# Kernel tuning notes

Hardware: AMD Instinct MI355X
Metric: run time of the kernel (lower is better)

## Reference

```python
import jax, jax.numpy as jnp
import numpy as np

N = 50000
IN_C, HID_C, OUT_C = 128, 64, 32
E = 800000
NEG_SLOPE = 0.2


def setup_inputs() -> dict:
    key = jax.random.key(0)
    ks = jax.random.split(key, 8)
    x = jax.random.normal(ks[0], (N, IN_C), dtype=jnp.float32)
    edge_index = jax.random.randint(ks[1], (2, E), 0, N, dtype=jnp.int64)
    # GATConv params (heads=1): lin weight, att_src/att_dst vectors, bias
    sc = 1.0 / np.sqrt(IN_C)
    W = jax.random.uniform(ks[2], (IN_C, HID_C), jnp.float32, -sc, sc)
    att_src = jax.random.normal(ks[3], (HID_C,), jnp.float32) * (1.0 / np.sqrt(HID_C))
    att_dst = jax.random.normal(ks[4], (HID_C,), jnp.float32) * (1.0 / np.sqrt(HID_C))
    bias_conv = jnp.zeros((HID_C,), jnp.float32)
    sl = 1.0 / np.sqrt(HID_C)
    W_lin = jax.random.uniform(ks[5], (HID_C, OUT_C), jnp.float32, -sl, sl)
    b_lin = jax.random.uniform(ks[6], (OUT_C,), jnp.float32, -sl, sl)
    return {"x": x, "edge_index": edge_index, "W": W, "att_src": att_src,
            "att_dst": att_dst, "bias_conv": bias_conv, "W_lin": W_lin, "b_lin": b_lin}


def reference(x, edge_index, W, att_src, att_dst, bias_conv, W_lin, b_lin):
    n = x.shape[0]
    h = x @ W  # [N, HID]
    # add self-loops (PyG GATConv default add_self_loops=True)
    loop = jnp.arange(n, dtype=edge_index.dtype)
    src = jnp.concatenate([edge_index[0], loop])  # [E+N]
    dst = jnp.concatenate([edge_index[1], loop])
    a_src = h @ att_src  # [N]
    a_dst = h @ att_dst
    e = jax.nn.leaky_relu(a_src[src] + a_dst[dst], NEG_SLOPE)  # [E+N]
    # segment softmax over incoming edges per destination node
    m = jax.ops.segment_max(e, dst, num_segments=n)
    e = jnp.exp(e - m[dst])
    denom = jax.ops.segment_sum(e, dst, num_segments=n)
    alpha = e / (denom[dst] + 1e-16)
    msg = alpha[:, None] * h[src]  # [E+N, HID]
    out = jax.ops.segment_sum(msg, dst, num_segments=n) + bias_conv
    out = jax.nn.relu(out)
    return out @ W_lin + b_lin
```

## Files before the change

### kernel.cpp

```cpp
#include <hip/hip_runtime.h>
#include <hip/hip_bf16.h>

#define IN_C  128
#define HID_C 64
#define OUT_C 32
#define NEG_SLOPE 0.2f
#define EPB1    8192
#define BUCKETW 64
#define RCAP    1536
#define NBKT    1024
#define CSTRIDE 16
#define XS_LD   136

typedef short bf16x8 __attribute__((ext_vector_type(8)));
typedef float f32x4  __attribute__((ext_vector_type(4)));

__device__ __forceinline__ unsigned short f2bf(float f) {
    __hip_bfloat16 h = __float2bfloat16(f);
    return *(unsigned short*)&h;
}
__device__ __forceinline__ float bflo(unsigned int u) {
    return __uint_as_float(u << 16);
}
__device__ __forceinline__ float bfhi(unsigned int u) {
    return __uint_as_float(u & 0xffff0000u);
}

__global__ __launch_bounds__(512) void gemm_bin1_kernel(
    const float* __restrict__ x, const float* __restrict__ W,
    const float* __restrict__ att_src, const float* __restrict__ att_dst,
    __hip_bfloat16* __restrict__ hb,
    float* __restrict__ a_src, float* __restrict__ a_dst,
    const int* __restrict__ ei, int E,
    int* __restrict__ bcur, unsigned* __restrict__ bucketbuf,
    int ngemm, int n_nodes)
{
    __shared__ __align__(16) unsigned char smem[52224];
    const int t = threadIdx.x;

    if ((int)blockIdx.x < ngemm) {
        unsigned short* xs = (unsigned short*)smem;
        unsigned short* wt = (unsigned short*)(smem + 34816);
        const int wv   = t >> 6;
        const int lane = t & 63;
        const int m16  = lane & 15;
        const int quad = lane >> 4;
        const int node0 = blockIdx.x * 128;
        const int nrows = min(128, n_nodes - node0);

        {
            const float4* xg = (const float4*)(x + (long)node0 * IN_C);
#pragma unroll
            for (int i = t; i < 4096; i += 512) {
                const int row = i >> 5;
                const int c4  = i & 31;
                float4 v = (row < nrows) ? xg[i] : make_float4(0.f, 0.f, 0.f, 0.f);
                ushort4 u;
                u.x = f2bf(v.x); u.y = f2bf(v.y);
                u.z = f2bf(v.z); u.w = f2bf(v.w);
                *(ushort4*)(xs + row * XS_LD + c4 * 4) = u;
            }
        }
        {
#pragma unroll
            for (int i = t; i < 2048; i += 512) {
                const int k  = i >> 4;
                const int n0 = (i & 15) * 4;
                const float4 v = *(const float4*)(W + k * HID_C + n0);
                wt[(n0 + 0) * XS_LD + k] = f2bf(v.x);
                wt[(n0 + 1) * XS_LD + k] = f2bf(v.y);
                wt[(n0 + 2) * XS_LD + k] = f2bf(v.z);
                wt[(n0 + 3) * XS_LD + k] = f2bf(v.w);
            }
        }
        __syncthreads();

        const int myrow0 = wv * 16;
        bf16x8 A[4];
#pragma unroll
        for (int k0 = 0; k0 < 4; ++k0)
            A[k0] = *(const bf16x8*)(xs + (myrow0 + m16) * XS_LD + k0 * 32 + quad * 8);

        f32x4 C[4];
#pragma unroll
        for (int c = 0; c < 4; ++c) {
            C[c] = (f32x4){0.f, 0.f, 0.f, 0.f};
#pragma unroll
            for (int k0 = 0; k0 < 4; ++k0) {
                const bf16x8 B = *(const bf16x8*)(wt + (c * 16 + m16) * XS_LD + k0 * 32 + quad * 8);
                C[c] = __builtin_amdgcn_mfma_f32_16x16x32_bf16(A[k0], B, C[c], 0, 0, 0);
            }
        }

#pragma unroll
        for (int c = 0; c < 4; ++c) {
#pragma unroll
            for (int r = 0; r < 4; ++r)
                xs[(myrow0 + quad * 4 + r) * XS_LD + c * 16 + m16] = f2bf(C[c][r]);
        }

        {
            float ps[4] = {0.f, 0.f, 0.f, 0.f};
            float pd[4] = {0.f, 0.f, 0.f, 0.f};
#pragma unroll
            for (int c = 0; c < 4; ++c) {
                const float av = att_src[c * 16 + m16];
                const float dv = att_dst[c * 16 + m16];
#pragma unroll
                for (int r = 0; r < 4; ++r) {
                    ps[r] = fmaf(C[c][r], av, ps[r]);
                    pd[r] = fmaf(C[c][r], dv, pd[r]);
                }
            }
#pragma unroll
            for (int off = 1; off <= 8; off <<= 1) {
#pragma unroll
                for (int r = 0; r < 4; ++r) {
                    ps[r] += __shfl_xor(ps[r], off, 64);
                    pd[r] += __shfl_xor(pd[r], off, 64);
                }
            }
            if (m16 == 0) {
#pragma unroll
                for (int r = 0; r < 4; ++r) {
                    const int row = myrow0 + quad * 4 + r;
                    if (row < nrows) {
                        a_src[node0 + row] = ps[r];
                        a_dst[node0 + row] = pd[r];
                    }
                }
            }
        }
        __syncthreads();

        {
#pragma unroll
            for (int i = t; i < 1024; i += 512) {
                const int row = i >> 3;
                const int c8  = (i & 7) * 8;
                if (row < nrows) {
                    const uint4 v = *(const uint4*)(xs + row * XS_LD + c8);
                    *(uint4*)((unsigned short*)hb + (long)(node0 + row) * HID_C + c8) = v;
                }
            }
        }
    } else {
        unsigned* stage = (unsigned*)smem;
        int* excl = (int*)(smem + 32768);
        int* cur  = (int*)(smem + 36864);
        int* gpos = (int*)(smem + 40960);
        int* wsum = (int*)(smem + 45056);

        const int base = (blockIdx.x - ngemm) * EPB1;
        const int nedge = min(EPB1, E - base);
        const int lane = t & 63, wv = t >> 6;

        for (int i = t; i < NBKT; i += 512) excl[i] = 0;
        __syncthreads();

        for (int i = t; i < nedge; i += 512)
            atomicAdd(&excl[ei[E + base + i] >> 6], 1);
        __syncthreads();

        {
            const int b0 = t * 2;
            const int c0 = excl[b0], c1 = excl[b0 + 1];
            const int tsum = c0 + c1;
            int incl = tsum;
#pragma unroll
            for (int off = 1; off <= 32; off <<= 1) {
                int u = __shfl_up(incl, off, 64);
                if (lane >= off) incl += u;
            }
            if (lane == 63) wsum[wv] = incl;
            __syncthreads();
            int wbase = 0;
#pragma unroll
            for (int w = 0; w < 8; ++w) wbase += (w < wv) ? wsum[w] : 0;
            int run = wbase + (incl - tsum);
            excl[b0]     = run; cur[b0]     = run; run += c0;
            excl[b0 + 1] = run; cur[b0 + 1] = run;
        }
        __syncthreads();

        for (int i = t; i < nedge; i += 512) {
            const int s = ei[base + i];
            const int d = ei[E + base + i];
            const int b = d >> 6;
            const int pos = atomicAdd(&cur[b], 1);
            stage[pos] = (unsigned)s | ((unsigned)(d & 63) << 16)
                         | ((unsigned)b << 22);
        }
        __syncthreads();

        for (int b = t; b < NBKT; b += 512) {
            const int c = cur[b] - excl[b];
            gpos[b] = (c > 0) ? atomicAdd(&bcur[b * CSTRIDE], c) : 0;
        }
        __syncthreads();

        for (int i = t; i < nedge; i += 512) {
            const unsigned r = stage[i];
            const int b = r >> 22;
            const int dp = gpos[b] + (i - excl[b]);
            if (dp < RCAP) bucketbuf[(long)b * RCAP + dp] = r & 0x3FFFFFu;
        }
    }
}

__global__ __launch_bounds__(512) void bucket_agg_kernel(
    const unsigned* __restrict__ bucketbuf, const int* __restrict__ bcursor,
    const __hip_bfloat16* __restrict__ hb,
    const float* __restrict__ a_src, const float* __restrict__ a_dst,
    const float* __restrict__ bias_conv,
    const float* __restrict__ W_lin, const float* __restrict__ b_lin,
    float* __restrict__ out, int n_nodes)
{
    __shared__ __align__(16) unsigned char smem[16384];
    unsigned* srtL = (unsigned*)smem;
    float*    srtW = (float*)(smem + 6144);
    int* cntd = (int*)(smem + 12288);
    int* rp   = (int*)(smem + 12544);
    int* curd = (int*)(smem + 12804);
    float* vvL = (float*)smem;

    const int t  = threadIdx.x;
    const int q  = blockIdx.x;
    const int d0 = q * BUCKETW;
    const int dmax = min(BUCKETW, n_nodes - d0);
    const int tot  = min(bcursor[q * CSTRIDE], RCAP);
    const int wv = t >> 6, lane = t & 63, g8 = lane >> 3, l = lane & 7;

    if (t < BUCKETW) cntd[t] = 0;
    __syncthreads();

    const unsigned* gsrc = bucketbuf + (long)q * RCAP;

    const int i0 = t, i1 = t + 512, i2 = t + 1024;
    const bool v0 = i0 < tot, v1 = i1 < tot, v2 = i2 < tot;
    const unsigned rr0 = v0 ? gsrc[i0] : 0u;
    const unsigned rr1 = v1 ? gsrc[i1] : 0u;
    const unsigned rr2 = v2 ? gsrc[i2] : 0u;
    const float as0 = v0 ? a_src[rr0 & 0xFFFF] : 0.f;
    const float as1 = v1 ? a_src[rr1 & 0xFFFF] : 0.f;
    const float as2 = v2 ? a_src[rr2 & 0xFFFF] : 0.f;
    const float ad0 = v0 ? a_dst[d0 + ((rr0 >> 16) & 63)] : 0.f;
    const float ad1 = v1 ? a_dst[d0 + ((rr1 >> 16) & 63)] : 0.f;
    const float ad2 = v2 ? a_dst[d0 + ((rr2 >> 16) & 63)] : 0.f;

    if (v0) atomicAdd(&cntd[(rr0 >> 16) & 63], 1);
    if (v1) atomicAdd(&cntd[(rr1 >> 16) & 63], 1);
    if (v2) atomicAdd(&cntd[(rr2 >> 16) & 63], 1);

    float ww0 = 0.f, ww1 = 0.f, ww2 = 0.f;
    if (v0) { float e = as0 + ad0; e = (e >= 0.f) ? e : NEG_SLOPE * e; ww0 = __expf(e); }
    if (v1) { float e = as1 + ad1; e = (e >= 0.f) ? e : NEG_SLOPE * e; ww1 = __expf(e); }
    if (v2) { float e = as2 + ad2; e = (e >= 0.f) ? e : NEG_SLOPE * e; ww2 = __expf(e); }
    __syncthreads();

    if (t < 64) {
        int c = cntd[t], incl = c;
#pragma unroll
        for (int off = 1; off <= 32; off <<= 1) {
            int u = __shfl_up(incl, off, 64);
            if (t >= off) incl += u;
        }
        rp[t] = incl - c;
        curd[t] = incl - c;
        if (t == 63) rp[64] = incl;
    }
    __syncthreads();

    if (v0) { const int p = atomicAdd(&curd[(rr0 >> 16) & 63], 1); srtL[p] = rr0; srtW[p] = ww0; }
    if (v1) { const int p = atomicAdd(&curd[(rr1 >> 16) & 63], 1); srtL[p] = rr1; srtW[p] = ww1; }
    if (v2) { const int p = atomicAdd(&curd[(rr2 >> 16) & 63], 1); srtL[p] = rr2; srtW[p] = ww2; }
    __syncthreads();

    const unsigned short* hbs = (const unsigned short*)hb;

    const int dloc = wv * 8 + g8;
    float vv[8];
#pragma unroll
    for (int kc = 0; kc < 8; ++kc) vv[kc] = 0.f;

    if (dloc < dmax) {
        const int d = d0 + dloc;
        float A[8];
        float den;
        {
            float e = a_src[d] + a_dst[d];
            e = (e >= 0.f) ? e : NEG_SLOPE * e;
            const float ws = __expf(e);
            const uint4 hv = *(const uint4*)(hbs + (long)d * HID_C + l * 8);
            den = ws;
            A[0] = ws * bflo(hv.x); A[1] = ws * bfhi(hv.x);
            A[2] = ws * bflo(hv.y); A[3] = ws * bfhi(hv.y);
            A[4] = ws * bflo(hv.z); A[5] = ws * bfhi(hv.z);
            A[6] = ws * bflo(hv.w); A[7] = ws * bfhi(hv.w);
        }
        const int beg = rp[dloc], fin = rp[dloc + 1];
        int j = beg;
        for (; j + 3 < fin; j += 4) {
            const unsigned r0 = srtL[j];
            const unsigned r1 = srtL[j + 1];
            const unsigned r2 = srtL[j + 2];
            const unsigned r3 = srtL[j + 3];
            const float w0 = srtW[j];
            const float w1 = srtW[j + 1];
            const float w2 = srtW[j + 2];
            const float w3 = srtW[j + 3];
            const uint4 h0 = *(const uint4*)(hbs + (long)(r0 & 0xFFFF) * HID_C + l * 8);
            const uint4 h1 = *(const uint4*)(hbs + (long)(r1 & 0xFFFF) * HID_C + l * 8);
            const uint4 h2 = *(const uint4*)(hbs + (long)(r2 & 0xFFFF) * HID_C + l * 8);
            const uint4 h3 = *(const uint4*)(hbs + (long)(r3 & 0xFFFF) * HID_C + l * 8);
            den += w0 + w1;
            den += w2 + w3;
            A[0] = fmaf(w0, bflo(h0.x), A[0]); A[1] = fmaf(w0, bfhi(h0.x), A[1]);
            A[2] = fmaf(w0, bflo(h0.y), A[2]); A[3] = fmaf(w0, bfhi(h0.y), A[3]);
            A[4] = fmaf(w0, bflo(h0.z), A[4]); A[5] = fmaf(w0, bfhi(h0.z), A[5]);
            A[6] = fmaf(w0, bflo(h0.w), A[6]); A[7] = fmaf(w0, bfhi(h0.w), A[7]);
            A[0] = fmaf(w1, bflo(h1.x), A[0]); A[1] = fmaf(w1, bfhi(h1.x), A[1]);
            A[2] = fmaf(w1, bflo(h1.y), A[2]); A[3] = fmaf(w1, bfhi(h1.y), A[3]);
            A[4] = fmaf(w1, bflo(h1.z), A[4]); A[5] = fmaf(w1, bfhi(h1.z), A[5]);
            A[6] = fmaf(w1, bflo(h1.w), A[6]); A[7] = fmaf(w1, bfhi(h1.w), A[7]);
            A[0] = fmaf(w2, bflo(h2.x), A[0]); A[1] = fmaf(w2, bfhi(h2.x), A[1]);
            A[2] = fmaf(w2, bflo(h2.y), A[2]); A[3] = fmaf(w2, bfhi(h2.y), A[3]);
            A[4] = fmaf(w2, bflo(h2.z), A[4]); A[5] = fmaf(w2, bfhi(h2.z), A[5]);
            A[6] = fmaf(w2, bflo(h2.w), A[6]); A[7] = fmaf(w2, bfhi(h2.w), A[7]);
            A[0] = fmaf(w3, bflo(h3.x), A[0]); A[1] = fmaf(w3, bfhi(h3.x), A[1]);
            A[2] = fmaf(w3, bflo(h3.y), A[2]); A[3] = fmaf(w3, bfhi(h3.y), A[3]);
            A[4] = fmaf(w3, bflo(h3.z), A[4]); A[5] = fmaf(w3, bfhi(h3.z), A[5]);
            A[6] = fmaf(w3, bflo(h3.w), A[6]); A[7] = fmaf(w3, bfhi(h3.w), A[7]);
        }
        for (; j < fin; ++j) {
            const unsigned r0 = srtL[j];
            const float    w0 = srtW[j];
            const uint4 h0 = *(const uint4*)(hbs + (long)(r0 & 0xFFFF) * HID_C + l * 8);
            den += w0;
            A[0] = fmaf(w0, bflo(h0.x), A[0]); A[1] = fmaf(w0, bfhi(h0.x), A[1]);
            A[2] = fmaf(w0, bflo(h0.y), A[2]); A[3] = fmaf(w0, bfhi(h0.y), A[3]);
            A[4] = fmaf(w0, bflo(h0.z), A[4]); A[5] = fmaf(w0, bfhi(h0.z), A[5]);
            A[6] = fmaf(w0, bflo(h0.w), A[6]); A[7] = fmaf(w0, bfhi(h0.w), A[7]);
        }
        const float rd = 1.0f / (den + 1e-16f);
#pragma unroll
        for (int kc = 0; kc < 8; ++kc) {
            float v = fmaf(A[kc], rd, bias_conv[l * 8 + kc]);
            vv[kc] = v > 0.f ? v : 0.f;
        }
    }

    __syncthreads();

    *(float4*)(vvL + dloc * HID_C + l * 8)     = make_float4(vv[0], vv[1], vv[2], vv[3]);
    *(float4*)(vvL + dloc * HID_C + l * 8 + 4) = make_float4(vv[4], vv[5], vv[6], vv[7]);
    __syncthreads();

    float Wr[8][4];
#pragma unroll
    for (int kc = 0; kc < 8; ++kc)
#pragma unroll
        for (int kj = 0; kj < 4; ++kj)
            Wr[kc][kj] = W_lin[(l * 8 + kc) * OUT_C + g8 * 4 + kj];
    float blinR[4];
#pragma unroll
    for (int kj = 0; kj < 4; ++kj) blinR[kj] = b_lin[g8 * 4 + kj];

    for (int dl = wv; dl < dmax; dl += 8) {
        const float4 va = *(const float4*)(vvL + dl * HID_C + l * 8);
        const float4 vb = *(const float4*)(vvL + dl * HID_C + l * 8 + 4);
        const float vvr[8] = {va.x, va.y, va.z, va.w, vb.x, vb.y, vb.z, vb.w};
        float p0 = 0.f, p1 = 0.f, p2 = 0.f, p3 = 0.f;
#pragma unroll
        for (int kc = 0; kc < 8; ++kc) {
            p0 = fmaf(vvr[kc], Wr[kc][0], p0);
            p1 = fmaf(vvr[kc], Wr[kc][1], p1);
            p2 = fmaf(vvr[kc], Wr[kc][2], p2);
            p3 = fmaf(vvr[kc], Wr[kc][3], p3);
        }
#pragma unroll
        for (int off = 1; off <= 4; off <<= 1) {
            p0 += __shfl_xor(p0, off, 64);
            p1 += __shfl_xor(p1, off, 64);
            p2 += __shfl_xor(p2, off, 64);
            p3 += __shfl_xor(p3, off, 64);
        }
        if (l == 0) {
            float4 o = make_float4(p0 + blinR[0], p1 + blinR[1],
                                   p2 + blinR[2], p3 + blinR[3]);
            *(float4*)(out + (long)(d0 + dl) * OUT_C + g8 * 4) = o;
        }
    }
}

extern "C" void kernel_launch(void* const* d_in, const int* in_sizes, int n_in,
                              void* d_out, int out_size, void* d_ws, size_t ws_size,
                              hipStream_t stream) {
    const float* x         = (const float*)d_in[0];
    const int*   ei        = (const int*)d_in[1];
    const float* W         = (const float*)d_in[2];
    const float* att_src   = (const float*)d_in[3];
    const float* att_dst   = (const float*)d_in[4];
    const float* bias_conv = (const float*)d_in[5];
    const float* W_lin     = (const float*)d_in[6];
    const float* b_lin     = (const float*)d_in[7];
    float*       out       = (float*)d_out;

    const int n_nodes = in_sizes[0] / IN_C;
    const int E       = in_sizes[1] / 2;
    const int B1   = (E + EPB1 - 1) / EPB1;
    const int Q    = (n_nodes + BUCKETW - 1) / BUCKETW;
    const int NG   = (n_nodes + 127) / 128;

    __hip_bfloat16* hb = (__hip_bfloat16*)d_ws;
    float* a_src   = (float*)(hb + (long)n_nodes * HID_C);
    float* a_dst   = a_src + n_nodes;
    int*   bcur    = (int*)(a_dst + n_nodes);
    unsigned* bucketbuf = (unsigned*)(bcur + (long)Q * CSTRIDE);

    hipMemsetAsync(bcur, 0, (size_t)Q * CSTRIDE * sizeof(int), stream);

    gemm_bin1_kernel<<<NG + B1, 512, 0, stream>>>(
        x, W, att_src, att_dst, hb, a_src, a_dst,
        ei, E, bcur, bucketbuf, NG, n_nodes);

    bucket_agg_kernel<<<Q, 512, 0, stream>>>(
        bucketbuf, bcur, hb, a_src, a_dst,
        bias_conv, W_lin, b_lin, out, n_nodes);
}
```

Baseline: 131.8 us.

## Load GEMM A-fragments directly from global, shrink LDS, cache edges in registers

The GEMM path now reads x rows straight from global memory into MFMA A-fragments instead of staging them through LDS, and reuses a smaller LDS region for W and the output tile. The binning path halves edges per block and keeps src/dst in registers between the counting and scatter passes, so edge_index is read from global only once. Together these cut LDS from about 52KB to 28KB to allow more resident blocks and remove redundant global reads. The cost is uncoalesced per-lane global loads for A, more binning blocks, and more global atomics on bucket counters.

Result: no change. 133.1 us (+1.0%).

```diff
diff --git a/kernel.cpp b/kernel.cpp
--- a/kernel.cpp
+++ b/kernel.cpp
@@ -5,12 +5,13 @@
 #define HID_C 64
 #define OUT_C 32
 #define NEG_SLOPE 0.2f
-#define EPB1    8192
+#define EPB1    4096
 #define BUCKETW 64
 #define RCAP    1536
 #define NBKT    1024
 #define CSTRIDE 16
 #define XS_LD   136
+#define CS_LD   72
 
 typedef short bf16x8 __attribute__((ext_vector_type(8)));
 typedef float f32x4  __attribute__((ext_vector_type(4)));
@@ -35,32 +36,20 @@
     int* __restrict__ bcur, unsigned* __restrict__ bucketbuf,
     int ngemm, int n_nodes)
 {
-    __shared__ __align__(16) unsigned char smem[52224];
+    __shared__ __align__(16) unsigned char smem[28704];
     const int t = threadIdx.x;
 
     if ((int)blockIdx.x < ngemm) {
-        unsigned short* xs = (unsigned short*)smem;
-        unsigned short* wt = (unsigned short*)(smem + 34816);
+        unsigned short* wt = (unsigned short*)smem;
+        unsigned short* cs = (unsigned short*)smem;
         const int wv   = t >> 6;
         const int lane = t & 63;
         const int m16  = lane & 15;
         const int quad = lane >> 4;
         const int node0 = blockIdx.x * 128;
         const int nrows = min(128, n_nodes - node0);
-
-        {
-            const float4* xg = (const float4*)(x + (long)node0 * IN_C);
-#pragma unroll
-            for (int i = t; i < 4096; i += 512) {
-                const int row = i >> 5;
-                const int c4  = i & 31;
-                float4 v = (row < nrows) ? xg[i] : make_float4(0.f, 0.f, 0.f, 0.f);
-                ushort4 u;
-                u.x = f2bf(v.x); u.y = f2bf(v.y);
-                u.z = f2bf(v.z); u.w = f2bf(v.w);
-                *(ushort4*)(xs + row * XS_LD + c4 * 4) = u;
-            }
-        }
+        const int myrow0 = wv * 16;
+
         {
 #pragma unroll
             for (int i = t; i < 2048; i += 512) {
@@ -73,13 +62,22 @@
                 wt[(n0 + 3) * XS_LD + k] = f2bf(v.w);
             }
         }
-        __syncthreads();
-
-        const int myrow0 = wv * 16;
+
+        const int arow = myrow0 + m16;
+        const float* xrow = x + (long)(node0 + ((arow < nrows) ? arow : 0)) * IN_C;
         bf16x8 A[4];
 #pragma unroll
-        for (int k0 = 0; k0 < 4; ++k0)
-            A[k0] = *(const bf16x8*)(xs + (myrow0 + m16) * XS_LD + k0 * 32 + quad * 8);
+        for (int k0 = 0; k0 < 4; ++k0) {
+            const float4 va = *(const float4*)(xrow + k0 * 32 + quad * 8);
+            const float4 vb = *(const float4*)(xrow + k0 * 32 + quad * 8 + 4);
+            bf16x8 a;
+            a[0] = (short)f2bf(va.x); a[1] = (short)f2bf(va.y);
+            a[2] = (short)f2bf(va.z); a[3] = (short)f2bf(va.w);
+            a[4] = (short)f2bf(vb.x); a[5] = (short)f2bf(vb.y);
+            a[6] = (short)f2bf(vb.z); a[7] = (short)f2bf(vb.w);
+            A[k0] = a;
+        }
+        __syncthreads();
 
         f32x4 C[4];
 #pragma unroll
@@ -90,13 +88,6 @@
                 const bf16x8 B = *(const bf16x8*)(wt + (c * 16 + m16) * XS_LD + k0 * 32 + quad * 8);
                 C[c] = __builtin_amdgcn_mfma_f32_16x16x32_bf16(A[k0], B, C[c], 0, 0, 0);
             }
-        }
-
-#pragma unroll
-        for (int c = 0; c < 4; ++c) {
-#pragma unroll
-            for (int r = 0; r < 4; ++r)
-                xs[(myrow0 + quad * 4 + r) * XS_LD + c * 16 + m16] = f2bf(C[c][r]);
         }
 
         {
@@ -131,6 +122,15 @@
                 }
             }
         }
+
+        __syncthreads();
+
+#pragma unroll
+        for (int c = 0; c < 4; ++c) {
+#pragma unroll
+            for (int r = 0; r < 4; ++r)
+                cs[(myrow0 + quad * 4 + r) * CS_LD + c * 16 + m16] = f2bf(C[c][r]);
+        }
         __syncthreads();
 
         {
@@ -139,17 +139,17 @@
                 const int row = i >> 3;
                 const int c8  = (i & 7) * 8;
                 if (row < nrows) {
-                    const uint4 v = *(const uint4*)(xs + row * XS_LD + c8);
+                    const uint4 v = *(const uint4*)(cs + row * CS_LD + c8);
                     *(uint4*)((unsigned short*)hb + (long)(node0 + row) * HID_C + c8) = v;
                 }
             }
         }
     } else {
         unsigned* stage = (unsigned*)smem;
-        int* excl = (int*)(smem + 32768);
-        int* cur  = (int*)(smem + 36864);
-        int* gpos = (int*)(smem + 40960);
-        int* wsum = (int*)(smem + 45056);
+        int* excl = (int*)(smem + 16384);
+        int* cur  = (int*)(smem + 20480);
+        int* gpos = (int*)(smem + 24576);
+        int* wsum = (int*)(smem + 28672);
 
         const int base = (blockIdx.x - ngemm) * EPB1;
         const int nedge = min(EPB1, E - base);
@@ -158,8 +158,15 @@
         for (int i = t; i < NBKT; i += 512) excl[i] = 0;
         __syncthreads();
 
-        for (int i = t; i < nedge; i += 512)
-            atomicAdd(&excl[ei[E + base + i] >> 6], 1);
+        int sreg[8], dreg[8];
+#pragma unroll
+        for (int k = 0; k < 8; ++k) {
+            const int i = t + k * 512;
+            const bool ok = i < nedge;
+            sreg[k] = ok ? ei[base + i] : 0;
+            dreg[k] = ok ? ei[E + base + i] : -1;
+            if (ok) atomicAdd(&excl[dreg[k] >> 6], 1);
+        }
         __syncthreads();
 
         {
@@ -183,13 +190,14 @@
         }
         __syncthreads();
 
-        for (int i = t; i < nedge; i += 512) {
-            const int s = ei[base + i];
-            const int d = ei[E + base + i];
-            const int b = d >> 6;
-            const int pos = atomicAdd(&cur[b], 1);
-            stage[pos] = (unsigned)s | ((unsigned)(d & 63) << 16)
-                         | ((unsigned)b << 22);
+#pragma unroll
+        for (int k = 0; k < 8; ++k) {
+            if (dreg[k] >= 0) {
+                const int b = dreg[k] >> 6;
+                const int pos = atomicAdd(&cur[b], 1);
+                stage[pos] = (unsigned)sreg[k] | ((unsigned)(dreg[k] & 63) << 16)
+                             | ((unsigned)b << 22);
+            }
         }
         __syncthreads();
 
```
